# Optimization experiments

Hardware: AMD Instinct MI355X
Metric: run time of the kernel (lower is better)

The kernel has to match this reference:

```python
import jax, jax.numpy as jnp
import numpy as np

B = 4            # batch
L = 4096         # max_len
D_MODEL = 1024   # qkv_dim == out_features
H = 16           # num_heads
SEG = 64         # max_seg_len
HD = D_MODEL // H          # head_dim = 64
NSEG = L // SEG            # num segments = 64
NEG = -1e10


def setup_inputs() -> dict:
    key = jax.random.key(0)
    k0, k1, k2, k3, k4 = jax.random.split(key, 5)
    scale = 1.0 / np.sqrt(D_MODEL).astype(np.float32)
    x = jax.random.normal(k0, (B, L, D_MODEL), jnp.float32)
    wq = jax.random.normal(k1, (D_MODEL, H, HD), jnp.float32) * scale
    wk = jax.random.normal(k2, (D_MODEL, H, HD), jnp.float32) * scale
    wv = jax.random.normal(k3, (D_MODEL, H, HD), jnp.float32) * scale
    wo = jax.random.normal(k4, (H, HD, D_MODEL), jnp.float32) * scale
    return {"input_qkv": x, "wq": wq, "wk": wk, "wv": wv, "wo": wo}


def reference(input_qkv, wq, wk, wv, wo):
    inv_sqrt_hd = 1.0 / np.sqrt(HD).astype(np.float32)
    # QKV projections; query pre-scaled by 1/sqrt(head_dim) as in get_qkv
    q = jnp.einsum('bld,dhf->blhf', input_qkv, wq) * inv_sqrt_hd
    k = jnp.einsum('bld,dhf->blhf', input_qkv, wk)
    v = jnp.einsum('bld,dhf->blhf', input_qkv, wv)

    cq = q.reshape(B * NSEG, SEG, H, HD)
    ck = k.reshape(B * NSEG, SEG, H, HD)
    cv = v.reshape(B * NSEG, SEG, H, HD)

    # Pooled per-segment query attends over its own segment's keys/values.
    # Original: merged_query = max(cq)*sqrt(HD), then flax dot_product_attention
    # rescales by 1/sqrt(HD) -> the two scalings cancel, so use max(cq) directly.
    mq = jnp.max(cq, axis=1, keepdims=True)                    # [B*NSEG, 1, H, HD]
    s_logits = jnp.einsum('bqhd,bkhd->bhqk', mq, ck)
    s_w = jax.nn.softmax(s_logits, axis=-1)
    s = jnp.einsum('bhqk,bkhd->bqhd', s_w, cv)                  # [B*NSEG, 1, H, HD]
    span_val = s.reshape(B, NSEG, H, HD)
    span_key = jnp.max(ck, axis=1).reshape(B, NSEG, H, HD)

    # Local causal attention logits within each segment
    causal = jnp.tril(jnp.ones((SEG, SEG), bool))
    local_bias = jnp.where(causal, 0.0, NEG).astype(jnp.float32)[None, :, None, :]
    local_logits = jnp.einsum('bqhd,bkhd->bqhk', cq, ck) + local_bias
    local_logits = local_logits.reshape(B, L, H, SEG)

    # Cross-segment logits: each token attends to strictly earlier segment summaries
    seg_id = jnp.arange(NSEG)
    prev_bias = jnp.where(seg_id[:, None] > seg_id[None, :], 0.0, NEG).astype(jnp.float32)
    prev_bias = jnp.repeat(prev_bias, SEG, axis=0)[None, :, None, :]  # [1, L, 1, NSEG]
    prev_logits = jnp.einsum('bqhd,bkhd->bqhk', q, span_key) + prev_bias

    # Joint softmax over [local keys | previous-segment summaries]
    joint = jnp.concatenate([local_logits, prev_logits], axis=-1)   # [B, L, H, SEG+NSEG]
    w = jax.nn.softmax(joint, axis=-1)
    local_att = w[..., :SEG].reshape(B * NSEG, SEG, H, SEG)
    prev_att = w[..., SEG:]

    local_merged = jnp.einsum('bqhk,bkhd->bqhd', local_att, cv).reshape(B, L, H, HD)
    prev_merged = jnp.einsum('bqhk,bkhd->bqhd', prev_att, span_val)

    return jnp.einsum('blhd,hdf->blf', local_merged + prev_merged, wo)
```

## Files before the change

kernel.cpp:

```cpp
#include <hip/hip_runtime.h>

#define BB    4
#define LL    4096
#define DM    1024
#define HH    16
#define SEGC  64
#define HDC   64
#define NSEGC 64
#define NEGV  -1.0e10f

typedef __bf16 bf16x8 __attribute__((ext_vector_type(8)));
typedef float  f32x4  __attribute__((ext_vector_type(4)));

__device__ __forceinline__ float bf2f(unsigned short s) {
  union { unsigned int u; float f; } x; x.u = ((unsigned int)s) << 16; return x.f;
}
__device__ __forceinline__ unsigned short f2bf(float f) {
  union { float f; unsigned int u; } x; x.f = f;
  unsigned int u = x.u;
  return (unsigned short)((u + 0x7fffu + ((u >> 16) & 1u)) >> 16);
}

__device__ __forceinline__ void gl2lds16(const unsigned short* g, unsigned short* l) {
  __builtin_amdgcn_global_load_lds(
      (const __attribute__((address_space(1))) unsigned int*)g,
      (__attribute__((address_space(3))) unsigned int*)l,
      16, 0, 0);
}

__device__ __forceinline__ void g2lds16(unsigned short* dst, const unsigned short* src) {
  int4 a = *(const int4*)(src);
  int4 b = *(const int4*)(src + 8);
  unsigned int* d = (unsigned int*)dst;
  const unsigned int* pa = (const unsigned int*)&a;
  const unsigned int* pb = (const unsigned int*)&b;
  d[0]=pa[0]; d[1]=pa[1]; d[2]=pa[2]; d[3]=pa[3];
  d[4]=pb[0]; d[5]=pb[1]; d[6]=pb[2]; d[7]=pb[3];
}

__global__ __launch_bounds__(256) void cvt_x(const float* __restrict__ x,
                                             unsigned short* __restrict__ xb) {
  const size_t i = ((size_t)blockIdx.x * 256 + threadIdx.x) * 8;
  float4 a = *(const float4*)(x + i);
  float4 b = *(const float4*)(x + i + 4);
  unsigned short o[8];
  o[0]=f2bf(a.x); o[1]=f2bf(a.y); o[2]=f2bf(a.z); o[3]=f2bf(a.w);
  o[4]=f2bf(b.x); o[5]=f2bf(b.y); o[6]=f2bf(b.z); o[7]=f2bf(b.w);
  *(int4*)(xb + i) = *(const int4*)o;
}

__global__ __launch_bounds__(256) void transpose_w(
    const float* __restrict__ wq, const float* __restrict__ wk,
    const float* __restrict__ wv, const float* __restrict__ wo,
    unsigned short* __restrict__ WqkvT, unsigned short* __restrict__ woT) {
  __shared__ unsigned short TS[64 * 65];

  const int z  = blockIdx.z;
  const int bx = blockIdx.x;
  const int by = blockIdx.y;
  const int t  = threadIdx.x;

  const float* src; unsigned short* dst; float scale = 1.0f;
  if (z == 0)      { src = wq; dst = WqkvT;               scale = 0.125f; }
  else if (z == 1) { src = wk; dst = WqkvT + 1024 * 1024; }
  else if (z == 2) { src = wv; dst = WqkvT + 2048 * 1024; }
  else             { src = wo; dst = woT; }

  const int rr = t >> 4;
  const int c4 = (t & 15) * 4;
  #pragma unroll
  for (int it = 0; it < 4; it++) {
    const int r = it * 16 + rr;
    float4 f = *(const float4*)(src + (size_t)(by * 64 + r) * 1024 + bx * 64 + c4);
    TS[(c4 + 0) * 65 + r] = f2bf(f.x * scale);
    TS[(c4 + 1) * 65 + r] = f2bf(f.y * scale);
    TS[(c4 + 2) * 65 + r] = f2bf(f.z * scale);
    TS[(c4 + 3) * 65 + r] = f2bf(f.w * scale);
  }
  __syncthreads();

  const int wr = t >> 3;
  const int w8 = (t & 7) * 8;
  #pragma unroll
  for (int it = 0; it < 2; it++) {
    const int n = it * 32 + wr;
    unsigned short o[8];
    #pragma unroll
    for (int j = 0; j < 8; j++) o[j] = TS[n * 65 + w8 + j];
    *(int4*)(dst + (size_t)(bx * 64 + n) * 1024 + by * 64 + w8) = *(const int4*)o;
  }
}

template <bool C_F32>
__global__ __launch_bounds__(256) void gemm_bt(
    const unsigned short* __restrict__ A,
    const unsigned short* __restrict__ Bt,
    void* __restrict__ Cv,
    int ldc)
{
  __shared__ __align__(16) unsigned short As[128 * 32];
  __shared__ __align__(16) unsigned short Bs[128 * 32];

  const int t    = threadIdx.x;
  const int wave = t >> 6;
  const int lane = t & 63;
  const int l15  = lane & 15;
  const int q4   = lane >> 4;
  const int wm   = wave >> 1;
  const int wn   = wave & 1;
  const int m0   = blockIdx.x * 128;
  const int n0   = blockIdx.y * 128;

  const int srow = lane >> 2;
  const int scol = (lane & 3) * 8;

  f32x4 acc[4][4];
  #pragma unroll
  for (int i = 0; i < 4; i++)
    #pragma unroll
    for (int j = 0; j < 4; j++)
      acc[i][j] = (f32x4){0.f, 0.f, 0.f, 0.f};

  for (int k0 = 0; k0 < 1024; k0 += 32) {
    __syncthreads();
    #pragma unroll
    for (int i = 0; i < 2; i++) {
      const int c = wave * 2 + i;
      gl2lds16(A  + (size_t)(m0 + c * 16 + srow) * 1024 + k0 + scol, As + c * 512);
      gl2lds16(Bt + (size_t)(n0 + c * 16 + srow) * 1024 + k0 + scol, Bs + c * 512);
    }
    __syncthreads();

    bf16x8 af[4], bfr[4];
    #pragma unroll
    for (int i = 0; i < 4; i++)
      af[i] = *(const bf16x8*)(As + (wm * 64 + i * 16 + l15) * 32 + q4 * 8);
    #pragma unroll
    for (int j = 0; j < 4; j++)
      bfr[j] = *(const bf16x8*)(Bs + (wn * 64 + j * 16 + l15) * 32 + q4 * 8);
    #pragma unroll
    for (int i = 0; i < 4; i++)
      #pragma unroll
      for (int j = 0; j < 4; j++)
        acc[i][j] = __builtin_amdgcn_mfma_f32_16x16x32_bf16(af[i], bfr[j], acc[i][j], 0, 0, 0);
  }

  #pragma unroll
  for (int i = 0; i < 4; i++) {
    #pragma unroll
    for (int j = 0; j < 4; j++) {
      const int col = n0 + wn * 64 + j * 16 + l15;
      #pragma unroll
      for (int r = 0; r < 4; r++) {
        const int row = m0 + wm * 64 + i * 16 + q4 * 4 + r;
        if (C_F32) ((float*)Cv)[(size_t)row * ldc + col] = acc[i][j][r];
        else ((unsigned short*)Cv)[(size_t)row * ldc + col] = f2bf(acc[i][j][r]);
      }
    }
  }
}

__global__ __launch_bounds__(64) void span_kernel(
    const unsigned short* __restrict__ qkv,
    unsigned short* __restrict__ spanK,
    unsigned short* __restrict__ spanV)
{
  __shared__ unsigned short QS[64 * 66], KS[64 * 66], VS[64 * 66];
  __shared__ float mqs[64], ws[64];

  const int c = blockIdx.x;
  const int h = blockIdx.y;
  const int b = c >> 6, n = c & 63;
  const int t = threadIdx.x;

  const size_t rowbase = ((size_t)(b * LL + n * SEGC + t)) * 3072 + h * 64;
  #pragma unroll
  for (int j = 0; j < 4; j++) {
    g2lds16(QS + t * 66 + j * 16, qkv + rowbase + j * 16);
    g2lds16(KS + t * 66 + j * 16, qkv + rowbase + 1024 + j * 16);
    g2lds16(VS + t * 66 + j * 16, qkv + rowbase + 2048 + j * 16);
  }
  __syncthreads();

  float mq = -3.0e38f, sk = -3.0e38f;
  for (int r = 0; r < 64; r++) {
    mq = fmaxf(mq, bf2f(QS[r * 66 + t]));
    sk = fmaxf(sk, bf2f(KS[r * 66 + t]));
  }
  mqs[t] = mq;
  spanK[((size_t)c * 16 + h) * 64 + t] = f2bf(sk);
  __syncthreads();

  float logit = 0.f;
  for (int d = 0; d < 64; d++) logit += mqs[d] * bf2f(KS[t * 66 + d]);
  float m = logit;
  #pragma unroll
  for (int off = 32; off; off >>= 1) m = fmaxf(m, __shfl_xor(m, off, 64));
  float e = __expf(logit - m);
  float s = e;
  #pragma unroll
  for (int off = 32; off; off >>= 1) s += __shfl_xor(s, off, 64);
  ws[t] = e / s;
  __syncthreads();

  float sv = 0.f;
  for (int kk = 0; kk < 64; kk++) sv += ws[kk] * bf2f(VS[kk * 66 + t]);
  spanV[((size_t)c * 16 + h) * 64 + t] = f2bf(sv);
}

__global__ __launch_bounds__(256) void attn_kernel(
    const unsigned short* __restrict__ qkv,
    const unsigned short* __restrict__ spanK,
    const unsigned short* __restrict__ spanV,
    unsigned short* __restrict__ att)
{
  __shared__ unsigned short VT[64 * 136];
  __shared__ unsigned short WL[64 * 136];

  const int c = blockIdx.x;
  const int h = blockIdx.y;
  const int b = c >> 6, n = c & 63;
  const int t = threadIdx.x;
  const int wave = t >> 6;
  const int lane = t & 63;
  const int l15  = lane & 15;
  const int q4   = lane >> 4;

  #pragma unroll
  for (int it = 0; it < 4; it++) {
    const int idx = t + 256 * it;
    const int kp  = idx >> 3;
    const int fc  = (idx & 7) * 8;
    const unsigned short* src;
    if (kp < 64)
      src = qkv + ((size_t)(b * LL + n * SEGC + kp)) * 3072 + 2048 + h * 64 + fc;
    else
      src = spanV + ((size_t)(b * 64 + (kp - 64)) * 16 + h) * 64 + fc;
    int4 val = *(const int4*)src;
    const unsigned short* e = (const unsigned short*)&val;
    #pragma unroll
    for (int i = 0; i < 8; i++) VT[(fc + i) * 136 + kp] = e[i];
  }

  bf16x8 af[2];
  {
    const size_t qbase = ((size_t)(b * LL + n * SEGC + wave * 16 + l15)) * 3072
                         + h * 64 + q4 * 8;
    af[0] = *(const bf16x8*)(qkv + qbase);
    af[1] = *(const bf16x8*)(qkv + qbase + 32);
  }

  f32x4 accl[8];
  #pragma unroll
  for (int tt = 0; tt < 8; tt++) accl[tt] = (f32x4){0.f, 0.f, 0.f, 0.f};

  #pragma unroll
  for (int s = 0; s < 2; s++) {
    bf16x8 bfr[8];
    #pragma unroll
    for (int tt = 0; tt < 8; tt++) {
      const unsigned short* src;
      if (tt < 4)
        src = qkv + ((size_t)(b * LL + n * SEGC + tt * 16 + l15)) * 3072
              + 1024 + h * 64 + s * 32 + q4 * 8;
      else
        src = spanK + ((size_t)((b * 64 + (tt - 4) * 16 + l15) * 16 + h)) * 64
              + s * 32 + q4 * 8;
      bfr[tt] = *(const bf16x8*)src;
    }
    #pragma unroll
    for (int tt = 0; tt < 8; tt++)
      accl[tt] = __builtin_amdgcn_mfma_f32_16x16x32_bf16(af[s], bfr[tt], accl[tt], 0, 0, 0);
  }

  #pragma unroll
  for (int tt = 0; tt < 8; tt++) {
    const int col = (tt & 3) * 16 + l15;
    #pragma unroll
    for (int rr = 0; rr < 4; rr++) {
      const int r_att = wave * 16 + q4 * 4 + rr;
      const bool valid = (tt < 4) ? (col <= r_att) : (col < n);
      if (!valid) accl[tt][rr] = NEGV;
    }
  }

  #pragma unroll
  for (int rr = 0; rr < 4; rr++) {
    float mx = accl[0][rr];
    #pragma unroll
    for (int tt = 1; tt < 8; tt++) mx = fmaxf(mx, accl[tt][rr]);
    #pragma unroll
    for (int msk = 1; msk < 16; msk <<= 1) mx = fmaxf(mx, __shfl_xor(mx, msk, 64));
    float sm = 0.f;
    float ex[8];
    #pragma unroll
    for (int tt = 0; tt < 8; tt++) { ex[tt] = __expf(accl[tt][rr] - mx); sm += ex[tt]; }
    #pragma unroll
    for (int msk = 1; msk < 16; msk <<= 1) sm += __shfl_xor(sm, msk, 64);
    const float inv = 1.0f / sm;
    const int r_att = wave * 16 + q4 * 4 + rr;
    #pragma unroll
    for (int tt = 0; tt < 8; tt++) {
      const int colj = (tt < 4) ? (tt * 16 + l15) : (64 + (tt - 4) * 16 + l15);
      WL[r_att * 136 + colj] = f2bf(ex[tt] * inv);
    }
  }

  __syncthreads();

  f32x4 accm[4];
  #pragma unroll
  for (int j = 0; j < 4; j++) accm[j] = (f32x4){0.f, 0.f, 0.f, 0.f};
  #pragma unroll
  for (int s = 0; s < 4; s++) {
    const bf16x8 aw = *(const bf16x8*)(WL + (wave * 16 + l15) * 136 + s * 32 + q4 * 8);
    #pragma unroll
    for (int j = 0; j < 4; j++) {
      const bf16x8 bv = *(const bf16x8*)(VT + (j * 16 + l15) * 136 + s * 32 + q4 * 8);
      accm[j] = __builtin_amdgcn_mfma_f32_16x16x32_bf16(aw, bv, accm[j], 0, 0, 0);
    }
  }

  #pragma unroll
  for (int j = 0; j < 4; j++) {
    #pragma unroll
    for (int rr = 0; rr < 4; rr++) {
      const int row = wave * 16 + q4 * 4 + rr;
      const int col = j * 16 + l15;
      att[((size_t)(b * LL + n * SEGC + row)) * 1024 + h * 64 + col] = f2bf(accm[j][rr]);
    }
  }
}

extern "C" void kernel_launch(void* const* d_in, const int* in_sizes, int n_in,
                              void* d_out, int out_size, void* d_ws, size_t ws_size,
                              hipStream_t stream) {
  const float* x  = (const float*)d_in[0];
  const float* wq = (const float*)d_in[1];
  const float* wk = (const float*)d_in[2];
  const float* wv = (const float*)d_in[3];
  const float* wo = (const float*)d_in[4];
  float* out = (float*)d_out;

  unsigned short* wsp   = (unsigned short*)d_ws;
  unsigned short* xb    = wsp;
  unsigned short* qkv   = xb + 16777216;
  unsigned short* WqkvT = qkv + 50331648;
  unsigned short* woT   = WqkvT + 3145728;
  unsigned short* skb   = woT + 1048576;
  unsigned short* svb   = skb + 262144;
  unsigned short* attb  = xb;

  cvt_x<<<8192, 256, 0, stream>>>(x, xb);
  transpose_w<<<dim3(16, 16, 4), 256, 0, stream>>>(wq, wk, wv, wo, WqkvT, woT);
  gemm_bt<false><<<dim3(128, 24), 256, 0, stream>>>(xb, WqkvT, (void*)qkv, 3072);
  span_kernel<<<dim3(256, 16), 64, 0, stream>>>(qkv, skb, svb);
  attn_kernel<<<dim3(256, 16), 256, 0, stream>>>(qkv, skb, svb, attb);
  gemm_bt<true><<<dim3(128, 8), 256, 0, stream>>>(attb, woT, (void*)out, 1024);
}
```

Before: 369.7 us.

## Replace GEMM with 256x256-tile double-buffered pipelined MFMA kernel

Replaces the 128x128 single-buffered GEMM with a 512-thread, 256x256-tile kernel. It double-buffers LDS with interleaved global-to-LDS loads, XOR-swizzles LDS addresses, raises wave priority around MFMA bursts and swizzles workgroup order for L2 locality. Both the QKV projection and the output projection use it. The aim is to hide load latency behind MFMAs and raise operand reuse, at the cost of larger LDS and register use, fewer workgroups, and a hand-tuned barrier and waitcnt schedule that is easy to get wrong.

After: 344.0 us. 7.0% less time.

```diff
diff --git a/kernel.cpp b/kernel.cpp
--- a/kernel.cpp
+++ b/kernel.cpp
@@ -92,72 +92,207 @@
 }
 
 template <bool C_F32>
-__global__ __launch_bounds__(256) void gemm_bt(
+__global__ __launch_bounds__(512, 2) void gemm256(
     const unsigned short* __restrict__ A,
     const unsigned short* __restrict__ Bt,
     void* __restrict__ Cv,
     int ldc)
 {
-  __shared__ __align__(16) unsigned short As[128 * 32];
-  __shared__ __align__(16) unsigned short Bs[128 * 32];
+  __shared__ __align__(16) unsigned short L[2][2][4][4096];
 
   const int t    = threadIdx.x;
   const int wave = t >> 6;
   const int lane = t & 63;
   const int l15  = lane & 15;
   const int q4   = lane >> 4;
-  const int wm   = wave >> 1;
-  const int wn   = wave & 1;
-  const int m0   = blockIdx.x * 128;
-  const int n0   = blockIdx.y * 128;
-
-  const int srow = lane >> 2;
-  const int scol = (lane & 3) * 8;
-
-  f32x4 acc[4][4];
-  #pragma unroll
-  for (int i = 0; i < 4; i++)
-    #pragma unroll
-    for (int j = 0; j < 4; j++)
-      acc[i][j] = (f32x4){0.f, 0.f, 0.f, 0.f};
-
-  for (int k0 = 0; k0 < 1024; k0 += 32) {
-    __syncthreads();
-    #pragma unroll
-    for (int i = 0; i < 2; i++) {
-      const int c = wave * 2 + i;
-      gl2lds16(A  + (size_t)(m0 + c * 16 + srow) * 1024 + k0 + scol, As + c * 512);
-      gl2lds16(Bt + (size_t)(n0 + c * 16 + srow) * 1024 + k0 + scol, Bs + c * 512);
-    }
-    __syncthreads();
-
-    bf16x8 af[4], bfr[4];
-    #pragma unroll
-    for (int i = 0; i < 4; i++)
-      af[i] = *(const bf16x8*)(As + (wm * 64 + i * 16 + l15) * 32 + q4 * 8);
-    #pragma unroll
-    for (int j = 0; j < 4; j++)
-      bfr[j] = *(const bf16x8*)(Bs + (wn * 64 + j * 16 + l15) * 32 + q4 * 8);
-    #pragma unroll
-    for (int i = 0; i < 4; i++)
-      #pragma unroll
-      for (int j = 0; j < 4; j++)
-        acc[i][j] = __builtin_amdgcn_mfma_f32_16x16x32_bf16(af[i], bfr[j], acc[i][j], 0, 0, 0);
-  }
-
-  #pragma unroll
-  for (int i = 0; i < 4; i++) {
-    #pragma unroll
-    for (int j = 0; j < 4; j++) {
+  const int wm   = wave >> 2;
+  const int wn   = wave & 3;
+
+  const int nwg = gridDim.x;
+  const int wg  = blockIdx.x;
+  const int swz = (wg & 7) * (nwg >> 3) + (wg >> 3);
+  const int m0  = (swz & 63) << 8;
+  const int n0  = (swz >> 6) << 8;
+
+  const int srow = ((wave >> 1) << 4) + (lane >> 2);
+  const int scol = ((wave & 1) << 5) + (((lane & 3) << 3) ^ (((lane >> 5) & 1) << 4));
+  const size_t laneoff = (size_t)srow * 1024 + scol;
+  const unsigned short* Ab = A  + (size_t)m0 * 1024 + laneoff;
+  const unsigned short* Bb = Bt + (size_t)n0 * 1024 + laneoff;
+
+  const int rdoff = l15 * 32 + ((q4 * 8) ^ (((l15 >> 3) & 1) << 4));
+
+#define SA_(d, q, kt) gl2lds16(Ab + ((size_t)(q) * 64) * 1024 + (size_t)(kt) * 64, \
+                               &L[d][0][q][0] + wave * 512)
+#define SB_(d, q, kt) gl2lds16(Bb + ((size_t)(q) * 64) * 1024 + (size_t)(kt) * 64, \
+                               &L[d][1][q][0] + wave * 512)
+#define LDA8(d, i, kk) (*(const bf16x8*)(&L[d][0][wm * 2 + ((i) >> 2)][0] + \
+                        ((((i) & 3) * 2 + (kk)) * 512) + rdoff))
+#define LDB8(d, j, kk) (*(const bf16x8*)(&L[d][1][wn][0] + \
+                        ((((j) * 2 + (kk))) * 512) + rdoff))
+#define BAR()   asm volatile("s_barrier" ::: "memory")
+#define LGKM0() asm volatile("s_waitcnt lgkmcnt(0)" ::: "memory")
+#define VMW(n)  asm volatile("s_waitcnt vmcnt(" #n ")" ::: "memory")
+#define MFMA_(av, bv, cv) __builtin_amdgcn_mfma_f32_16x16x32_bf16(av, bv, cv, 0, 0, 0)
+
+  f32x4 acc[8][4];
+  #pragma unroll
+  for (int i = 0; i < 8; ++i)
+    #pragma unroll
+    for (int j = 0; j < 4; ++j) acc[i][j] = (f32x4){0.f, 0.f, 0.f, 0.f};
+
+  SB_(0,0,0); SB_(0,1,0); SB_(0,2,0); SB_(0,3,0); SA_(0,0,0); SA_(0,2,0);
+  SA_(0,1,0); SA_(0,3,0);
+  SB_(1,0,1); SB_(1,1,1); SB_(1,2,1); SB_(1,3,1); SA_(1,0,1); SA_(1,2,1);
+  VMW(8); BAR();
+
+  #pragma unroll 1
+  for (int it = 0; it < 8; ++it) {
+    const int t1 = 2 * it + 1;
+    const int s2 = (2 * it + 2) & 15;
+    const int s3 = (2 * it + 3) & 15;
+    bf16x8 a[4][2], b[4][2];
+
+    #pragma unroll
+    for (int ii = 0; ii < 4; ++ii) { a[ii][0] = LDA8(0, ii, 0); a[ii][1] = LDA8(0, ii, 1); }
+    #pragma unroll
+    for (int jj = 0; jj < 4; ++jj) { b[jj][0] = LDB8(0, jj, 0); b[jj][1] = LDB8(0, jj, 1); }
+    SA_(1, 1, t1); SA_(1, 3, t1);
+    BAR(); LGKM0();
+    __builtin_amdgcn_s_setprio(1);
+    #pragma unroll
+    for (int ii = 0; ii < 4; ++ii)
+      #pragma unroll
+      for (int jj = 0; jj < 2; ++jj) {
+        acc[ii][jj] = MFMA_(a[ii][0], b[jj][0], acc[ii][jj]);
+        acc[ii][jj] = MFMA_(a[ii][1], b[jj][1], acc[ii][jj]);
+      }
+    __builtin_amdgcn_s_setprio(0);
+    BAR();
+
+    SB_(0, 0, s2); SB_(0, 1, s2);
+    BAR();
+    __builtin_amdgcn_s_setprio(1);
+    #pragma unroll
+    for (int ii = 0; ii < 4; ++ii)
+      #pragma unroll
+      for (int jj = 2; jj < 4; ++jj) {
+        acc[ii][jj] = MFMA_(a[ii][0], b[jj][0], acc[ii][jj]);
+        acc[ii][jj] = MFMA_(a[ii][1], b[jj][1], acc[ii][jj]);
+      }
+    __builtin_amdgcn_s_setprio(0);
+    VMW(10); BAR();
+
+    #pragma unroll
+    for (int ii = 0; ii < 4; ++ii) { a[ii][0] = LDA8(0, 4 + ii, 0); a[ii][1] = LDA8(0, 4 + ii, 1); }
+    SB_(0, 2, s2); SB_(0, 3, s2);
+    BAR(); LGKM0();
+    __builtin_amdgcn_s_setprio(1);
+    #pragma unroll
+    for (int ii = 0; ii < 4; ++ii)
+      #pragma unroll
+      for (int jj = 2; jj < 4; ++jj) {
+        acc[4 + ii][jj] = MFMA_(a[ii][0], b[jj][0], acc[4 + ii][jj]);
+        acc[4 + ii][jj] = MFMA_(a[ii][1], b[jj][1], acc[4 + ii][jj]);
+      }
+    __builtin_amdgcn_s_setprio(0);
+    BAR();
+
+    SA_(0, 0, s2); SA_(0, 2, s2);
+    BAR();
+    __builtin_amdgcn_s_setprio(1);
+    #pragma unroll
+    for (int ii = 0; ii < 4; ++ii)
+      #pragma unroll
+      for (int jj = 0; jj < 2; ++jj) {
+        acc[4 + ii][jj] = MFMA_(a[ii][0], b[jj][0], acc[4 + ii][jj]);
+        acc[4 + ii][jj] = MFMA_(a[ii][1], b[jj][1], acc[4 + ii][jj]);
+      }
+    __builtin_amdgcn_s_setprio(0);
+    VMW(8); BAR();
+
+    #pragma unroll
+    for (int ii = 0; ii < 4; ++ii) { a[ii][0] = LDA8(1, ii, 0); a[ii][1] = LDA8(1, ii, 1); }
+    #pragma unroll
+    for (int jj = 0; jj < 4; ++jj) { b[jj][0] = LDB8(1, jj, 0); b[jj][1] = LDB8(1, jj, 1); }
+    SA_(0, 1, s2); SA_(0, 3, s2);
+    BAR(); LGKM0();
+    __builtin_amdgcn_s_setprio(1);
+    #pragma unroll
+    for (int ii = 0; ii < 4; ++ii)
+      #pragma unroll
+      for (int jj = 0; jj < 2; ++jj) {
+        acc[ii][jj] = MFMA_(a[ii][0], b[jj][0], acc[ii][jj]);
+        acc[ii][jj] = MFMA_(a[ii][1], b[jj][1], acc[ii][jj]);
+      }
+    __builtin_amdgcn_s_setprio(0);
+    BAR();
+
+    SB_(1, 0, s3); SB_(1, 1, s3);
+    BAR();
+    __builtin_amdgcn_s_setprio(1);
+    #pragma unroll
+    for (int ii = 0; ii < 4; ++ii)
+      #pragma unroll
+      for (int jj = 2; jj < 4; ++jj) {
+        acc[ii][jj] = MFMA_(a[ii][0], b[jj][0], acc[ii][jj]);
+        acc[ii][jj] = MFMA_(a[ii][1], b[jj][1], acc[ii][jj]);
+      }
+    __builtin_amdgcn_s_setprio(0);
+    VMW(10); BAR();
+
+    #pragma unroll
+    for (int ii = 0; ii < 4; ++ii) { a[ii][0] = LDA8(1, 4 + ii, 0); a[ii][1] = LDA8(1, 4 + ii, 1); }
+    SB_(1, 2, s3); SB_(1, 3, s3);
+    BAR(); LGKM0();
+    __builtin_amdgcn_s_setprio(1);
+    #pragma unroll
+    for (int ii = 0; ii < 4; ++ii)
+      #pragma unroll
+      for (int jj = 2; jj < 4; ++jj) {
+        acc[4 + ii][jj] = MFMA_(a[ii][0], b[jj][0], acc[4 + ii][jj]);
+        acc[4 + ii][jj] = MFMA_(a[ii][1], b[jj][1], acc[4 + ii][jj]);
+      }
+    __builtin_amdgcn_s_setprio(0);
+    BAR();
+
+    SA_(1, 0, s3); SA_(1, 2, s3);
+    BAR();
+    __builtin_amdgcn_s_setprio(1);
+    #pragma unroll
+    for (int ii = 0; ii < 4; ++ii)
+      #pragma unroll
+      for (int jj = 0; jj < 2; ++jj) {
+        acc[4 + ii][jj] = MFMA_(a[ii][0], b[jj][0], acc[4 + ii][jj]);
+        acc[4 + ii][jj] = MFMA_(a[ii][1], b[jj][1], acc[4 + ii][jj]);
+      }
+    __builtin_amdgcn_s_setprio(0);
+    VMW(8); BAR();
+  }
+
+  #pragma unroll
+  for (int i = 0; i < 8; ++i) {
+    #pragma unroll
+    for (int j = 0; j < 4; ++j) {
       const int col = n0 + wn * 64 + j * 16 + l15;
       #pragma unroll
-      for (int r = 0; r < 4; r++) {
-        const int row = m0 + wm * 64 + i * 16 + q4 * 4 + r;
+      for (int r = 0; r < 4; ++r) {
+        const int row = m0 + wm * 128 + i * 16 + q4 * 4 + r;
         if (C_F32) ((float*)Cv)[(size_t)row * ldc + col] = acc[i][j][r];
         else ((unsigned short*)Cv)[(size_t)row * ldc + col] = f2bf(acc[i][j][r]);
       }
     }
   }
+  VMW(0);
+
+#undef SA_
+#undef SB_
+#undef LDA8
+#undef LDB8
+#undef BAR
+#undef LGKM0
+#undef VMW
+#undef MFMA_
 }
 
 __global__ __launch_bounds__(64) void span_kernel(
@@ -353,8 +488,8 @@
 
   cvt_x<<<8192, 256, 0, stream>>>(x, xb);
   transpose_w<<<dim3(16, 16, 4), 256, 0, stream>>>(wq, wk, wv, wo, WqkvT, woT);
-  gemm_bt<false><<<dim3(128, 24), 256, 0, stream>>>(xb, WqkvT, (void*)qkv, 3072);
+  gemm256<false><<<768, 512, 0, stream>>>(xb, WqkvT, (void*)qkv, 3072);
   span_kernel<<<dim3(256, 16), 64, 0, stream>>>(qkv, skb, svb);
   attn_kernel<<<dim3(256, 16), 256, 0, stream>>>(qkv, skb, svb, attb);
-  gemm_bt<true><<<dim3(128, 8), 256, 0, stream>>>(attb, woT, (void*)out, 1024);
-}
+  gemm256<true><<<256, 512, 0, stream>>>(attb, woT, (void*)out, 1024);
+}
```
